# Kernel optimization log

Measured on AMD Instinct MI355X. Metric: run time of the kernel, lower is better.

The kernel has to match this reference:

```python
import jax, jax.numpy as jnp
import numpy as np

D_MODEL = 1024
N_HEADS = 16
HEAD_DIM = D_MODEL // N_HEADS
FFN = 4096
NUM_REL = 64
BATCH = 4
SEQ = 1024
EPS = 1e-6


def _layernorm(x, g, b):
    mu = jnp.mean(x, axis=-1, keepdims=True)
    var = jnp.mean(jnp.square(x - mu), axis=-1, keepdims=True)
    return (x - mu) * jax.lax.rsqrt(var + EPS) * g + b


def setup_inputs() -> dict:
    key = jax.random.key(0)
    ks = jax.random.split(key, 16)
    s_d = 1.0 / np.sqrt(D_MODEL)
    s_f = 1.0 / np.sqrt(FFN)
    inp = {
        "x": jax.random.normal(ks[0], (BATCH, SEQ, D_MODEL), jnp.float32),
        "relative_ids": jax.random.randint(ks[1], (SEQ, SEQ), 0, NUM_REL),
        # attention projections (row-major: y = x @ W + b)
        "Wq": jax.random.normal(ks[2], (D_MODEL, D_MODEL), jnp.float32) * s_d,
        "bq": jnp.zeros((D_MODEL,), jnp.float32),
        "Wk": jax.random.normal(ks[3], (D_MODEL, D_MODEL), jnp.float32) * s_d,
        "bk": jnp.zeros((D_MODEL,), jnp.float32),
        "Wv": jax.random.normal(ks[4], (D_MODEL, D_MODEL), jnp.float32) * s_d,
        "bv": jnp.zeros((D_MODEL,), jnp.float32),
        "Wo": jax.random.normal(ks[5], (D_MODEL, D_MODEL), jnp.float32) * s_d,
        "bo": jnp.zeros((D_MODEL,), jnp.float32),
        # relative position tables: Ek for keys (rel-e), Eb per-head bias (rel-b)
        "Ek": jax.random.normal(ks[6], (NUM_REL, HEAD_DIM), jnp.float32) * (1.0 / np.sqrt(HEAD_DIM)),
        "Eb": jax.random.normal(ks[7], (NUM_REL, N_HEADS), jnp.float32) * 0.02,
        # layernorms
        "g1": jnp.ones((D_MODEL,), jnp.float32),
        "b1": jnp.zeros((D_MODEL,), jnp.float32),
        "g2": jnp.ones((D_MODEL,), jnp.float32),
        "b2": jnp.zeros((D_MODEL,), jnp.float32),
        # FFN
        "W1": jax.random.normal(ks[8], (D_MODEL, FFN), jnp.float32) * s_d,
        "bf1": jnp.zeros((FFN,), jnp.float32),
        "W2": jax.random.normal(ks[9], (FFN, D_MODEL), jnp.float32) * s_f,
        "bf2": jnp.zeros((D_MODEL,), jnp.float32),
    }
    return inp


def _forward(x, relative_ids, Wq, bq, Wk, bk, Wv, bv, Wo, bo, Ek, Eb,
             g1, b1, g2, b2, W1, bf1, W2, bf2):
    B, S, D = x.shape
    # projections -> [B, H, S, Dh]
    def split_heads(t):
        return t.reshape(B, S, N_HEADS, HEAD_DIM).transpose(0, 2, 1, 3)
    q = split_heads(x @ Wq + bq)
    k = split_heads(x @ Wk + bk)
    v = split_heads(x @ Wv + bv)

    scores = jnp.einsum('bhqd,bhkd->bhqk', q, k)
    # rel-e: relative key embeddings interact with queries
    Erel = Ek[relative_ids]                      # [S, S, Dh]
    scores = scores + jnp.einsum('bhqd,qkd->bhqk', q, Erel)
    # rel-b: per-head relative bias
    scores = scores + Eb[relative_ids].transpose(2, 0, 1)[None]  # [1,H,S,S]
    scores = scores / jnp.sqrt(jnp.asarray(HEAD_DIM, x.dtype))

    attn = jax.nn.softmax(scores, axis=-1)
    ctx = jnp.einsum('bhqk,bhkd->bhqd', attn, v)
    ctx = ctx.transpose(0, 2, 1, 3).reshape(B, S, D)
    a_out = ctx @ Wo + bo

    # dropout is identity at eval
    ff_in = _layernorm(x + a_out, g1, b1)
    ff = jax.nn.relu(ff_in @ W1 + bf1) @ W2 + bf2
    return _layernorm(ff_in + ff, g2, b2)


def reference(x, relative_ids, Wq, bq, Wk, bk, Wv, bv, Wo, bo, Ek, Eb,
              g1, b1, g2, b2, W1, bf1, W2, bf2):
    return _forward(x, relative_ids, Wq, bq, Wk, bk, Wv, bv, Wo, bo, Ek, Eb,
                    g1, b1, g2, b2, W1, bf1, W2, bf2)
```

## Files before the change

### kernel.cpp

```cpp
#include <hip/hip_runtime.h>


typedef short bf16x8 __attribute__((ext_vector_type(8)));
typedef float f32x4 __attribute__((ext_vector_type(4)));

#define DEVI static __device__ __forceinline__

constexpr int SEQ = 1024, DMODEL = 1024, NH = 16, HDIM = 64, FFDIM = 4096, NREL = 64, NBATCH = 4;
constexpr int ROWS = NBATCH * SEQ;
#define QSC 0.18033688011112042f

DEVI unsigned short f2b(float f) {
  union { float f; unsigned u; } v; v.f = f;
  unsigned r = v.u + 0x7FFFu + ((v.u >> 16) & 1u);
  return (unsigned short)(r >> 16);
}

DEVI float b2f(unsigned short u) {
  union { unsigned v; float f; } x; x.v = (unsigned)u << 16; return x.f;
}

#if __has_builtin(__builtin_amdgcn_cvt_pk_bf16_f32)
DEVI unsigned pack2(float a, float b) {
  auto r = __builtin_amdgcn_cvt_pk_bf16_f32(a, b);
  return __builtin_bit_cast(unsigned, r);
}
#else
DEVI unsigned pack2(float a, float b) {
  return (unsigned)f2b(a) | ((unsigned)f2b(b) << 16);
}
#endif

DEVI float fexp2(float x) {
#if __has_builtin(__builtin_amdgcn_exp2f)
  return __builtin_amdgcn_exp2f(x);
#else
  return exp2f(x);
#endif
}

DEVI float4 ld4h(const unsigned short* p) {
  uint2 u = *(const uint2*)p;
  union { unsigned v; float f; } a, b, c, d;
  a.v = u.x << 16; b.v = u.x & 0xffff0000u; c.v = u.y << 16; d.v = u.y & 0xffff0000u;
  return make_float4(a.f, b.f, c.f, d.f);
}

DEVI void gload16(const unsigned short* g, unsigned short* l) {
  __builtin_amdgcn_global_load_lds((const __attribute__((address_space(1))) void*)g,
                                   (__attribute__((address_space(3))) void*)l, 16, 0, 0);
}

template <int BM, int BN>
DEVI void g256_core(const unsigned short* __restrict__ A, int lda,
                    const unsigned short* __restrict__ Bt, int ldb, int K,
                    unsigned short* S, f32x4* acc) {
  constexpr int MT = BM / 32, NT = BN / 64;
  constexpr int LOADS = BM / 64 + BN / 64;
  constexpr int SBUF = (BM + BN) * 64;
  const int tid = threadIdx.x, wave = tid >> 6, lane = tid & 63;
  const int wm = wave & 1, wn = wave >> 1;
  const int lr = lane & 15, kq = lane >> 4;
  const int srow = lane >> 3, schunk = (lane & 7) ^ (srow & 7);
  const int sw = lr & 7;

  const f32x4 zero = {0.f, 0.f, 0.f, 0.f};
#pragma unroll
  for (int i = 0; i < MT * NT; ++i) acc[i] = zero;

  const unsigned short* ga = A + (size_t)(wave * (BM / 8) + srow) * lda + schunk * 8;
  const unsigned short* gb = Bt + (size_t)(wave * (BN / 8) + srow) * ldb + schunk * 8;
  unsigned short* dA = S + wave * (BM / 8) * 64;
  unsigned short* dB = S + BM * 64 + wave * (BN / 8) * 64;

#define STG(buf, k0)                                                         \
  do {                                                                       \
    _Pragma("unroll") for (int j = 0; j < BM / 64; ++j)                      \
        gload16(ga + (size_t)(j * 8) * lda + (k0), dA + (buf)*SBUF + j * 8 * 64); \
    _Pragma("unroll") for (int j = 0; j < BN / 64; ++j)                      \
        gload16(gb + (size_t)(j * 8) * ldb + (k0), dB + (buf)*SBUF + j * 8 * 64); \
  } while (0)

  STG(0, 0);
  STG(1, 64);

  const unsigned short* pa = S + (wm * (BM / 2) + lr) * 64;
  const unsigned short* pb = S + BM * 64 + (wn * (BN / 4) + lr) * 64;
  const int nt = K >> 6;

  for (int t = 0; t < nt; ++t) {
    const int buf = t & 1;
    if (t < nt - 1) {
      if constexpr (LOADS == 8) {
        asm volatile("s_waitcnt vmcnt(8)" ::: "memory");
      } else {
        asm volatile("s_waitcnt vmcnt(6)" ::: "memory");
      }
    } else {
      asm volatile("s_waitcnt vmcnt(0)" ::: "memory");
    }
    __builtin_amdgcn_s_barrier();
    asm volatile("" ::: "memory");
    const unsigned short* qa = pa + buf * SBUF;
    const unsigned short* qb = pb + buf * SBUF;
#pragma unroll
    for (int ks = 0; ks < 2; ++ks) {
      const int rc = ((ks * 4 + kq) ^ sw) * 8;
      bf16x8 af[MT], bv[NT];
#pragma unroll
      for (int mi = 0; mi < MT; ++mi) af[mi] = *(const bf16x8*)(qa + mi * 16 * 64 + rc);
#pragma unroll
      for (int ni = 0; ni < NT; ++ni) bv[ni] = *(const bf16x8*)(qb + ni * 16 * 64 + rc);
#pragma unroll
      for (int mi = 0; mi < MT; ++mi)
#pragma unroll
        for (int ni = 0; ni < NT; ++ni)
          acc[mi * NT + ni] =
              __builtin_amdgcn_mfma_f32_16x16x32_bf16(af[mi], bv[ni], acc[mi * NT + ni], 0, 0, 0);
    }
    asm volatile("" ::: "memory");
    __builtin_amdgcn_s_barrier();
    asm volatile("" ::: "memory");
    if (t + 2 < nt) STG(buf, (t + 2) * 64);
  }
#undef STG
}

template <int BN2, bool RELU, bool SPLITK>
__global__ __launch_bounds__(512, 2) void k_g256(const unsigned short* __restrict__ A, int lda,
                                                 const unsigned short* __restrict__ Bt, int ldb,
                                                 int K, int N, const float* __restrict__ bias,
                                                 unsigned short* __restrict__ outh,
                                                 size_t ostride) {
  constexpr int BM = 256, MT = 8, NT = BN2 / 64;
  __shared__ __align__(16) unsigned short S[2 * (BM + BN2) * 64];
  f32x4 acc[MT * NT];
  const int m0 = blockIdx.y * BM, n0 = blockIdx.x * BN2;
  const int kc = SPLITK ? blockIdx.z : 0;
  g256_core<BM, BN2>(A + (size_t)m0 * lda + (size_t)kc * K, lda,
                     Bt + (size_t)n0 * ldb + (size_t)kc * K, ldb, K, S, acc);
  if (SPLITK) outh += (size_t)kc * ostride;
  const int tid = threadIdx.x, wave = tid >> 6, lane = tid & 63;
  const int wm = wave & 1, wn = wave >> 1, lr = lane & 15, kq = lane >> 4;
#pragma unroll
  for (int mi = 0; mi < MT; ++mi) {
    const int row0 = m0 + wm * 128 + mi * 16 + kq * 4;
#pragma unroll
    for (int ni = 0; ni < NT; ++ni) {
      const int col = n0 + wn * (BN2 / 4) + ni * 16 + lr;
      const float bc = (!SPLITK || kc == 0) ? bias[col] : 0.f;
      f32x4 v = acc[mi * NT + ni];
#pragma unroll
      for (int r = 0; r < 4; ++r) {
        float y = v[r] + bc;
        if (RELU) y = fmaxf(y, 0.f);
        outh[(size_t)(row0 + r) * N + col] = f2b(y);
      }
    }
  }
}

__global__ __launch_bounds__(512, 2) void k_proj256(
    const unsigned short* __restrict__ A, const unsigned short* __restrict__ WqT,
    const unsigned short* __restrict__ WkT, const unsigned short* __restrict__ WvT,
    const float* __restrict__ bq, const float* __restrict__ bk, const float* __restrict__ bv,
    unsigned short* __restrict__ oq, unsigned short* __restrict__ ok,
    unsigned short* __restrict__ ov) {
  __shared__ __align__(16) unsigned short S[2 * 512 * 64];
  f32x4 acc[32];
  const int which = blockIdx.z;
  const unsigned short* Bt = which == 0 ? WqT : which == 1 ? WkT : WvT;
  const float* bias = which == 0 ? bq : which == 1 ? bk : bv;
  unsigned short* out = which == 0 ? oq : which == 1 ? ok : ov;
  const float scl = which == 0 ? QSC : 1.0f;
  const int m0 = blockIdx.y * 256, n0 = blockIdx.x * 256;
  g256_core<256, 256>(A + (size_t)m0 * DMODEL, DMODEL, Bt + (size_t)n0 * DMODEL, DMODEL, DMODEL,
                      S, acc);
  const int tid = threadIdx.x, wave = tid >> 6, lane = tid & 63;
  const int wm = wave & 1, wn = wave >> 1, lr = lane & 15, kq = lane >> 4;
#pragma unroll
  for (int mi = 0; mi < 8; ++mi) {
    const int row0 = m0 + wm * 128 + mi * 16 + kq * 4;
    const int b = row0 >> 10, s0 = row0 & 1023;
#pragma unroll
    for (int ni = 0; ni < 4; ++ni) {
      const int col = n0 + wn * 64 + ni * 16 + lr;
      const int h = col >> 6, d = col & 63;
      const float bc = bias[col];
      f32x4 v = acc[mi * 4 + ni];
#pragma unroll
      for (int r = 0; r < 4; ++r) v[r] = (v[r] + bc) * scl;
      if (which != 2) {
#pragma unroll
        for (int r = 0; r < 4; ++r)
          out[((size_t)((b * NH + h) * SEQ) + s0 + r) * HDIM + d] = f2b(v[r]);
      } else {
        uint2 p = make_uint2(pack2(v[0], v[1]), pack2(v[2], v[3]));
        *(uint2*)&out[((size_t)((b * NH + h) * HDIM) + d) * SEQ + s0] = p;
      }
    }
  }
}

__global__ __launch_bounds__(256, 4) void k_flash(const unsigned short* __restrict__ q,
                                                  const unsigned short* __restrict__ kk,
                                                  const unsigned short* __restrict__ vT,
                                                  const unsigned short* __restrict__ Ekb,
                                                  const float* __restrict__ Eb,
                                                  const unsigned char* __restrict__ rel8,
                                                  unsigned short* __restrict__ ctx) {
  __shared__ __align__(16) unsigned short sK[128 * 64];
  __shared__ __align__(16) unsigned short sV[64 * 128];
  __shared__ __align__(16) unsigned short sqEB16[64 * 62];
  __shared__ float sRow[4][16];

  const int tid = threadIdx.x, wave = tid >> 6, lane = tid & 63;
  const int lr = lane & 15, kq = lane >> 4;

  const int L = blockIdx.y * 16 + blockIdx.x;
  const int xcd = L & 7, idx = L >> 3;
  const int z = xcd * 8 + (idx >> 4), qt = idx & 15;
  const int b = z >> 4, h = z & 15;
  const size_t zo = (size_t)z * SEQ * HDIM;
  const size_t vo = (size_t)z * HDIM * SEQ;

  const int srow8 = lane >> 3, sl8 = lane & 7;
  const int sw8 = sl8 ^ (srow8 & 7);
  const int dl = lane >> 4, sl16 = lane & 15;
  const int swl = lr & 7;
  const f32x4 zero = {0.f, 0.f, 0.f, 0.f};

  unsigned short* sQv = sV;
#pragma unroll
  for (int j = 0; j < 2; ++j) {
    const int row = wave * 16 + j * 8 + srow8;
    gload16(q + zo + (size_t)(qt * 64 + row) * 64 + sw8 * 8, sQv + (wave * 16 + j * 8) * 64);
    gload16(Ekb + (size_t)row * 64 + sw8 * 8, sK + (wave * 16 + j * 8) * 64);
  }
  __syncthreads();

  bf16x8 bq_[2];
#pragma unroll
  for (int ks = 0; ks < 2; ++ks)
    bq_[ks] = *(const bf16x8*)&sQv[(wave * 16 + lr) * 64 + (((ks * 4 + kq) ^ swl) << 3)];

  {
    f32x4 accE[4];
#pragma unroll
    for (int nf = 0; nf < 4; ++nf) accE[nf] = zero;
#pragma unroll
    for (int ks = 0; ks < 2; ++ks) {
#pragma unroll
      for (int nf = 0; nf < 4; ++nf) {
        bf16x8 ek = *(const bf16x8*)&sK[(nf * 16 + lr) * 64 + (((ks * 4 + kq) ^ swl) << 3)];
        accE[nf] = __builtin_amdgcn_mfma_f32_16x16x32_bf16(bq_[ks], ek, accE[nf], 0, 0, 0);
      }
    }
#pragma unroll
    for (int nf = 0; nf < 4; ++nf) {
      const int rid = nf * 16 + lr;
      const float eb = Eb[rid * NH + h] * QSC;
      const int base = rid * 62 + wave * 16 + kq * 4;
      *(unsigned*)&sqEB16[base] = pack2(accE[nf][0] + eb, accE[nf][1] + eb);
      *(unsigned*)&sqEB16[base + 2] = pack2(accE[nf][2] + eb, accE[nf][3] + eb);
    }
  }

  float l_run = 0.f;
  f32x4 accO[4];
#pragma unroll
  for (int nd = 0; nd < 4; ++nd) accO[nd] = zero;
  const int qrow_g = qt * 64 + wave * 16 + lr;
  const unsigned char* relrow8 = rel8 + (size_t)qrow_g * SEQ;
  const int qcol = wave * 16 + lr;
  unsigned short* sPw = sK + wave * 2048;

  for (int kt = 0; kt < 8; ++kt) {
    __syncthreads();
#pragma unroll
    for (int j = 0; j < 4; ++j) {
      const int row = wave * 32 + j * 8 + srow8;
      gload16(kk + zo + (size_t)(kt * 128 + row) * 64 + sw8 * 8, sK + (wave * 32 + j * 8) * 64);
    }
#pragma unroll
    for (int j = 0; j < 4; ++j) {
      const int row = wave * 16 + j * 4 + dl;
      const int ch = sl16 ^ (row & 15);
      gload16(vT + vo + (size_t)row * SEQ + kt * 128 + ch * 8, sV + (wave * 16 + j * 4) * 128);
    }
    unsigned ru[8];
#pragma unroll
    for (int mi = 0; mi < 8; ++mi)
      ru[mi] = *(const unsigned*)&relrow8[kt * 128 + mi * 16 + kq * 4];
    __syncthreads();

    f32x4 accS[8];
#pragma unroll
    for (int mi = 0; mi < 8; ++mi) accS[mi] = zero;
#pragma unroll
    for (int ks = 0; ks < 2; ++ks) {
#pragma unroll
      for (int mi = 0; mi < 8; ++mi) {
        bf16x8 a = *(const bf16x8*)&sK[(mi * 16 + lr) * 64 + (((ks * 4 + kq) ^ swl) << 3)];
        accS[mi] = __builtin_amdgcn_mfma_f32_16x16x32_bf16(a, bq_[ks], accS[mi], 0, 0, 0);
      }
    }
#pragma unroll
    for (int mi = 0; mi < 8; ++mi) {
      const float p0 = fexp2(accS[mi][0] + b2f(sqEB16[(int)(ru[mi] & 255u) * 62 + qcol]));
      const float p1 = fexp2(accS[mi][1] + b2f(sqEB16[(int)((ru[mi] >> 8) & 255u) * 62 + qcol]));
      const float p2 = fexp2(accS[mi][2] + b2f(sqEB16[(int)((ru[mi] >> 16) & 255u) * 62 + qcol]));
      const float p3 = fexp2(accS[mi][3] + b2f(sqEB16[(int)(ru[mi] >> 24) * 62 + qcol]));
      accS[mi][0] = p0; accS[mi][1] = p1; accS[mi][2] = p2; accS[mi][3] = p3;
      l_run += (p0 + p1) + (p2 + p3);
    }
    __syncthreads();

#pragma unroll
    for (int mi = 0; mi < 8; ++mi) {
      const int c = 2 * mi + (kq >> 1);
      *(uint2*)&sPw[lr * 128 + ((c ^ lr) << 3) + ((kq & 1) << 2)] =
          make_uint2(pack2(accS[mi][0], accS[mi][1]), pack2(accS[mi][2], accS[mi][3]));
    }
#pragma unroll
    for (int kst = 0; kst < 4; ++kst) {
      const int cc = ((kq + 4 * kst) ^ lr) << 3;
      bf16x8 a = *(const bf16x8*)&sPw[lr * 128 + cc];
#pragma unroll
      for (int nd = 0; nd < 4; ++nd) {
        bf16x8 bv = *(const bf16x8*)&sV[(nd * 16 + lr) * 128 + cc];
        accO[nd] = __builtin_amdgcn_mfma_f32_16x16x32_bf16(a, bv, accO[nd], 0, 0, 0);
      }
    }
  }

  l_run += __shfl_xor(l_run, 16);
  l_run += __shfl_xor(l_run, 32);
  if (kq == 0) sRow[wave][lr] = l_run;
  const float4 lv = *(const float4*)&sRow[wave][kq * 4];
  const float inv[4] = {1.f / lv.x, 1.f / lv.y, 1.f / lv.z, 1.f / lv.w};
  const size_t rbase = (size_t)(b * SEQ + qt * 64 + wave * 16 + kq * 4);
#pragma unroll
  for (int nd = 0; nd < 4; ++nd) {
    const int col = h * HDIM + nd * 16 + lr;
#pragma unroll
    for (int r = 0; r < 4; ++r)
      ctx[(rbase + r) * DMODEL + col] = f2b(accO[nd][r] * inv[r]);
  }
}

template <bool WB>
__global__ __launch_bounds__(256) void k_addln3(const unsigned short* __restrict__ a,
                                                const unsigned short* __restrict__ p0,
                                                const unsigned short* __restrict__ p1,
                                                const float* __restrict__ g,
                                                const float* __restrict__ beta,
                                                float* __restrict__ outf,
                                                unsigned short* __restrict__ outh) {
  const int row = blockIdx.x, t = threadIdx.x;
  const size_t base = (size_t)row * DMODEL + t * 4;
  float4 va = ld4h(&a[base]);
  float4 v0 = ld4h(&p0[base]);
  float4 v1 = ld4h(&p1[base]);
  const float x0 = va.x + v0.x + v1.x, x1 = va.y + v0.y + v1.y;
  const float x2 = va.z + v0.z + v1.z, x3 = va.w + v0.w + v1.w;
  __shared__ float red[4];
  float s = x0 + x1 + x2 + x3;
#pragma unroll
  for (int o = 32; o; o >>= 1) s += __shfl_xor(s, o);
  if ((t & 63) == 0) red[t >> 6] = s;
  __syncthreads();
  const float mu = (red[0] + red[1] + red[2] + red[3]) * (1.0f / DMODEL);
  __syncthreads();
  const float d0 = x0 - mu, d1 = x1 - mu, d2 = x2 - mu, d3 = x3 - mu;
  float qv = d0 * d0 + d1 * d1 + d2 * d2 + d3 * d3;
#pragma unroll
  for (int o = 32; o; o >>= 1) qv += __shfl_xor(qv, o);
  if ((t & 63) == 0) red[t >> 6] = qv;
  __syncthreads();
  const float var = (red[0] + red[1] + red[2] + red[3]) * (1.0f / DMODEL);
  const float sc = rsqrtf(var + 1e-6f);
  float4 vg = *(const float4*)&g[t * 4];
  float4 ve = *(const float4*)&beta[t * 4];
  float4 y;
  y.x = d0 * sc * vg.x + ve.x;
  y.y = d1 * sc * vg.y + ve.y;
  y.z = d2 * sc * vg.z + ve.z;
  y.w = d3 * sc * vg.w + ve.w;
  if (WB) {
    uint2 p = make_uint2(pack2(y.x, y.y), pack2(y.z, y.w));
    *(uint2*)&outh[base] = p;
  } else {
    *(float4*)&outf[base] = y;
  }
}

__global__ __launch_bounds__(256) void k_tcast12(
    const float* __restrict__ Wq, const float* __restrict__ Wk, const float* __restrict__ Wv,
    const float* __restrict__ Wo, const float* __restrict__ W1, const float* __restrict__ W2,
    unsigned short* __restrict__ oq, unsigned short* __restrict__ ok,
    unsigned short* __restrict__ ov, unsigned short* __restrict__ oo,
    unsigned short* __restrict__ o1, unsigned short* __restrict__ o2) {
  const int z = blockIdx.z;
  const float* in;
  unsigned short* out;
  int ldi, ldo;
  if (z < 4) {
    in = z == 0 ? Wq : z == 1 ? Wk : z == 2 ? Wv : Wo;
    out = z == 0 ? oq : z == 1 ? ok : z == 2 ? ov : oo;
    ldi = 1024; ldo = 1024;
  } else if (z < 8) {
    const int s = z - 4;
    in = W1 + (size_t)s * 1024; ldi = 4096;
    out = o1 + (size_t)s * 1024 * 1024; ldo = 1024;
  } else {
    const int s = z - 8;
    in = W2 + (size_t)s * 1024 * 1024; ldi = 1024;
    out = o2 + (size_t)s * 1024; ldo = 4096;
  }
  __shared__ float tile[32][33];
  const int tx = threadIdx.x & 31, ty = threadIdx.x >> 5;
  const int r0 = blockIdx.y * 32, c0 = blockIdx.x * 32;
#pragma unroll
  for (int i = 0; i < 4; ++i)
    tile[ty + i * 8][tx] = in[(size_t)(r0 + ty + i * 8) * ldi + c0 + tx];
  __syncthreads();
#pragma unroll
  for (int i = 0; i < 4; ++i)
    out[(size_t)(c0 + ty + i * 8) * ldo + r0 + tx] = f2b(tile[tx][ty + i * 8]);
}

__global__ __launch_bounds__(256) void k_cast2(const float* __restrict__ a,
                                               unsigned short* __restrict__ oa, int n4a,
                                               const float* __restrict__ bsrc,
                                               unsigned short* __restrict__ ob, int n4b,
                                               const int* __restrict__ rel,
                                               unsigned char* __restrict__ r8, int n4c) {
  const int i = blockIdx.x * 256 + threadIdx.x;
  if (i < n4a) {
    float4 v = *(const float4*)&a[(size_t)i * 4];
    uint2 p = make_uint2(pack2(v.x, v.y), pack2(v.z, v.w));
    *(uint2*)&oa[(size_t)i * 4] = p;
  } else {
    const int j = i - n4a;
    if (j < n4b) {
      float4 v = *(const float4*)&bsrc[(size_t)j * 4];
      uint2 p = make_uint2(pack2(v.x, v.y), pack2(v.z, v.w));
      *(uint2*)&ob[(size_t)j * 4] = p;
    } else {
      const int k2 = j - n4b;
      if (k2 < n4c) {
        int4 v = *(const int4*)&rel[(size_t)k2 * 4];
        unsigned pk = (unsigned)(v.x & 255) | ((unsigned)(v.y & 255) << 8) |
                      ((unsigned)(v.z & 255) << 16) | ((unsigned)(v.w & 255) << 24);
        *(unsigned*)&r8[(size_t)k2 * 4] = pk;
      }
    }
  }
}


extern "C" void kernel_launch(void* const* d_in, const int* in_sizes, int n_in, void* d_out,
                              int out_size, void* d_ws, size_t ws_size, hipStream_t stream) {
  const float* x = (const float*)d_in[0];
  const int* rel = (const int*)d_in[1];
  const float* Wq = (const float*)d_in[2];
  const float* bq = (const float*)d_in[3];
  const float* Wk = (const float*)d_in[4];
  const float* bk = (const float*)d_in[5];
  const float* Wv = (const float*)d_in[6];
  const float* bv = (const float*)d_in[7];
  const float* Wo = (const float*)d_in[8];
  const float* bo = (const float*)d_in[9];
  const float* Ek = (const float*)d_in[10];
  const float* Eb = (const float*)d_in[11];
  const float* g1 = (const float*)d_in[12];
  const float* b1 = (const float*)d_in[13];
  const float* g2 = (const float*)d_in[14];
  const float* b2 = (const float*)d_in[15];
  const float* W1 = (const float*)d_in[16];
  const float* bf1 = (const float*)d_in[17];
  const float* W2 = (const float*)d_in[18];
  const float* bf2 = (const float*)d_in[19];
  float* out = (float*)d_out;

  char* ws = (char*)d_ws;
  const size_t MB = 1ull << 20;
  unsigned short* Wqt = (unsigned short*)(ws + 0 * MB);
  unsigned short* Wkt = (unsigned short*)(ws + 2 * MB);
  unsigned short* Wvt = (unsigned short*)(ws + 4 * MB);
  unsigned short* Wot = (unsigned short*)(ws + 6 * MB);
  unsigned short* W1t = (unsigned short*)(ws + 8 * MB);
  unsigned short* W2t = (unsigned short*)(ws + 16 * MB);
  unsigned short* xb = (unsigned short*)(ws + 24 * MB);
  unsigned short* Ekb = (unsigned short*)(ws + 32 * MB);
  unsigned short* qbuf = (unsigned short*)(ws + 33 * MB);
  unsigned short* kbuf = (unsigned short*)(ws + 41 * MB);
  unsigned short* vTb = (unsigned short*)(ws + 49 * MB);
  unsigned short* ctx = (unsigned short*)(ws + 57 * MB);
  unsigned short* Pb = (unsigned short*)(ws + 65 * MB);
  unsigned char* rel8 = (unsigned char*)(ws + 65 * MB);
  unsigned short* ff_in_b = (unsigned short*)(ws + 81 * MB);
  unsigned short* hidden = (unsigned short*)(ws + 89 * MB);
  const size_t OST = (size_t)ROWS * DMODEL;

  k_tcast12<<<dim3(32, 32, 12), 256, 0, stream>>>(Wq, Wk, Wv, Wo, W1, W2, Wqt, Wkt, Wvt, Wot,
                                                  W1t, W2t);
  k_cast2<<<5124, 256, 0, stream>>>(x, xb, ROWS * DMODEL / 4, Ek, Ekb, NREL * HDIM / 4, rel, rel8,
                                    SEQ * SEQ / 4);

  k_proj256<<<dim3(4, 16, 3), 512, 0, stream>>>(xb, Wqt, Wkt, Wvt, bq, bk, bv, qbuf, kbuf, vTb);

  k_flash<<<dim3(16, 64), 256, 0, stream>>>(qbuf, kbuf, vTb, Ekb, Eb, rel8, ctx);

  k_g256<128, false, true><<<dim3(8, 16, 2), 512, 0, stream>>>(ctx, DMODEL, Wot, DMODEL,
                                                               DMODEL / 2, DMODEL, bo, Pb, OST);
  k_addln3<true><<<ROWS, 256, 0, stream>>>(xb, Pb, Pb + OST, g1, b1, nullptr, ff_in_b);

  k_g256<256, true, false><<<dim3(FFDIM / 256, ROWS / 256), 512, 0, stream>>>(
      ff_in_b, DMODEL, W1t, DMODEL, DMODEL, FFDIM, bf1, hidden, 0);
  k_g256<128, false, true><<<dim3(8, 16, 2), 512, 0, stream>>>(hidden, FFDIM, W2t, FFDIM,
                                                               FFDIM / 2, DMODEL, bf2, Pb, OST);
  k_addln3<false><<<ROWS, 256, 0, stream>>>(ff_in_b, Pb, Pb + OST, g2, b2, out, nullptr);
}
```

Before: 342.1 us.

## Pre-scale relative ids to byte offsets, add MFMA priority, split-K-4 on FFN down GEMM

The relative-id table is now stored as 16-bit values that are already scaled into byte offsets for the shared bias table. This removes the multiply-and-index work from the flash inner loop, but doubles the bytes read for rel ids. s_setprio is raised around the MFMA blocks in the attention kernel to favour matrix issue. The FFN down-projection changes from 2-way to 4-way split-K with 256-wide tiles, and a new add-layernorm kernel sums the four partials, trading more partial-sum traffic for better occupancy.

```diff
diff --git a/kernel.cpp b/kernel.cpp
--- a/kernel.cpp
+++ b/kernel.cpp
@@ -207,7 +207,7 @@
                                                   const unsigned short* __restrict__ vT,
                                                   const unsigned short* __restrict__ Ekb,
                                                   const float* __restrict__ Eb,
-                                                  const unsigned char* __restrict__ rel8,
+                                                  const unsigned short* __restrict__ rel16,
                                                   unsigned short* __restrict__ ctx) {
   __shared__ __align__(16) unsigned short sK[128 * 64];
   __shared__ __align__(16) unsigned short sV[64 * 128];
@@ -271,8 +271,9 @@
 #pragma unroll
   for (int nd = 0; nd < 4; ++nd) accO[nd] = zero;
   const int qrow_g = qt * 64 + wave * 16 + lr;
-  const unsigned char* relrow8 = rel8 + (size_t)qrow_g * SEQ;
+  const unsigned short* relrow16 = rel16 + (size_t)qrow_g * SEQ;
   const int qcol = wave * 16 + lr;
+  const char* sqb = (const char*)sqEB16 + 2 * qcol;
   unsigned short* sPw = sK + wave * 2048;
 
   for (int kt = 0; kt < 8; ++kt) {
@@ -288,15 +289,16 @@
       const int ch = sl16 ^ (row & 15);
       gload16(vT + vo + (size_t)row * SEQ + kt * 128 + ch * 8, sV + (wave * 16 + j * 4) * 128);
     }
-    unsigned ru[8];
+    uint2 ru[8];
 #pragma unroll
     for (int mi = 0; mi < 8; ++mi)
-      ru[mi] = *(const unsigned*)&relrow8[kt * 128 + mi * 16 + kq * 4];
+      ru[mi] = *(const uint2*)&relrow16[kt * 128 + mi * 16 + kq * 4];
     __syncthreads();
 
     f32x4 accS[8];
 #pragma unroll
     for (int mi = 0; mi < 8; ++mi) accS[mi] = zero;
+    __builtin_amdgcn_s_setprio(1);
 #pragma unroll
     for (int ks = 0; ks < 2; ++ks) {
 #pragma unroll
@@ -305,12 +307,13 @@
         accS[mi] = __builtin_amdgcn_mfma_f32_16x16x32_bf16(a, bq_[ks], accS[mi], 0, 0, 0);
       }
     }
+    __builtin_amdgcn_s_setprio(0);
 #pragma unroll
     for (int mi = 0; mi < 8; ++mi) {
-      const float p0 = fexp2(accS[mi][0] + b2f(sqEB16[(int)(ru[mi] & 255u) * 62 + qcol]));
-      const float p1 = fexp2(accS[mi][1] + b2f(sqEB16[(int)((ru[mi] >> 8) & 255u) * 62 + qcol]));
-      const float p2 = fexp2(accS[mi][2] + b2f(sqEB16[(int)((ru[mi] >> 16) & 255u) * 62 + qcol]));
-      const float p3 = fexp2(accS[mi][3] + b2f(sqEB16[(int)(ru[mi] >> 24) * 62 + qcol]));
+      const float p0 = fexp2(accS[mi][0] + b2f(*(const unsigned short*)(sqb + (ru[mi].x & 0xffffu))));
+      const float p1 = fexp2(accS[mi][1] + b2f(*(const unsigned short*)(sqb + (ru[mi].x >> 16))));
+      const float p2 = fexp2(accS[mi][2] + b2f(*(const unsigned short*)(sqb + (ru[mi].y & 0xffffu))));
+      const float p3 = fexp2(accS[mi][3] + b2f(*(const unsigned short*)(sqb + (ru[mi].y >> 16))));
       accS[mi][0] = p0; accS[mi][1] = p1; accS[mi][2] = p2; accS[mi][3] = p3;
       l_run += (p0 + p1) + (p2 + p3);
     }
@@ -322,6 +325,7 @@
       *(uint2*)&sPw[lr * 128 + ((c ^ lr) << 3) + ((kq & 1) << 2)] =
           make_uint2(pack2(accS[mi][0], accS[mi][1]), pack2(accS[mi][2], accS[mi][3]));
     }
+    __builtin_amdgcn_s_setprio(1);
 #pragma unroll
     for (int kst = 0; kst < 4; ++kst) {
       const int cc = ((kq + 4 * kst) ^ lr) << 3;
@@ -332,6 +336,7 @@
         accO[nd] = __builtin_amdgcn_mfma_f32_16x16x32_bf16(a, bv, accO[nd], 0, 0, 0);
       }
     }
+    __builtin_amdgcn_s_setprio(0);
   }
 
   l_run += __shfl_xor(l_run, 16);
@@ -393,6 +398,49 @@
   } else {
     *(float4*)&outf[base] = y;
   }
+}
+
+__global__ __launch_bounds__(256) void k_addln4(const unsigned short* __restrict__ a,
+                                                const unsigned short* __restrict__ p,
+                                                size_t ost,
+                                                const float* __restrict__ g,
+                                                const float* __restrict__ beta,
+                                                float* __restrict__ outf) {
+  const int row = blockIdx.x, t = threadIdx.x;
+  const size_t base = (size_t)row * DMODEL + t * 4;
+  float4 va = ld4h(&a[base]);
+  float4 v0 = ld4h(&p[base]);
+  float4 v1 = ld4h(&p[base + ost]);
+  float4 v2 = ld4h(&p[base + 2 * ost]);
+  float4 v3 = ld4h(&p[base + 3 * ost]);
+  const float x0 = va.x + (v0.x + v1.x) + (v2.x + v3.x);
+  const float x1 = va.y + (v0.y + v1.y) + (v2.y + v3.y);
+  const float x2 = va.z + (v0.z + v1.z) + (v2.z + v3.z);
+  const float x3 = va.w + (v0.w + v1.w) + (v2.w + v3.w);
+  __shared__ float red[4];
+  float s = x0 + x1 + x2 + x3;
+#pragma unroll
+  for (int o = 32; o; o >>= 1) s += __shfl_xor(s, o);
+  if ((t & 63) == 0) red[t >> 6] = s;
+  __syncthreads();
+  const float mu = (red[0] + red[1] + red[2] + red[3]) * (1.0f / DMODEL);
+  __syncthreads();
+  const float d0 = x0 - mu, d1 = x1 - mu, d2 = x2 - mu, d3 = x3 - mu;
+  float qv = d0 * d0 + d1 * d1 + d2 * d2 + d3 * d3;
+#pragma unroll
+  for (int o = 32; o; o >>= 1) qv += __shfl_xor(qv, o);
+  if ((t & 63) == 0) red[t >> 6] = qv;
+  __syncthreads();
+  const float var = (red[0] + red[1] + red[2] + red[3]) * (1.0f / DMODEL);
+  const float sc = rsqrtf(var + 1e-6f);
+  float4 vg = *(const float4*)&g[t * 4];
+  float4 ve = *(const float4*)&beta[t * 4];
+  float4 y;
+  y.x = d0 * sc * vg.x + ve.x;
+  y.y = d1 * sc * vg.y + ve.y;
+  y.z = d2 * sc * vg.z + ve.z;
+  y.w = d3 * sc * vg.w + ve.w;
+  *(float4*)&outf[base] = y;
 }
 
 __global__ __launch_bounds__(256) void k_tcast12(
@@ -435,7 +483,7 @@
                                                const float* __restrict__ bsrc,
                                                unsigned short* __restrict__ ob, int n4b,
                                                const int* __restrict__ rel,
-                                               unsigned char* __restrict__ r8, int n4c) {
+                                               unsigned short* __restrict__ r16, int n4c) {
   const int i = blockIdx.x * 256 + threadIdx.x;
   if (i < n4a) {
     float4 v = *(const float4*)&a[(size_t)i * 4];
@@ -451,9 +499,10 @@
       const int k2 = j - n4b;
       if (k2 < n4c) {
         int4 v = *(const int4*)&rel[(size_t)k2 * 4];
-        unsigned pk = (unsigned)(v.x & 255) | ((unsigned)(v.y & 255) << 8) |
-                      ((unsigned)(v.z & 255) << 16) | ((unsigned)(v.w & 255) << 24);
-        *(unsigned*)&r8[(size_t)k2 * 4] = pk;
+        uint2 pk;
+        pk.x = (unsigned)((v.x & 63) * 124) | ((unsigned)((v.y & 63) * 124) << 16);
+        pk.y = (unsigned)((v.z & 63) * 124) | ((unsigned)((v.w & 63) * 124) << 16);
+        *(uint2*)&r16[(size_t)k2 * 4] = pk;
       }
     }
   }
@@ -499,19 +548,20 @@
   unsigned short* vTb = (unsigned short*)(ws + 49 * MB);
   unsigned short* ctx = (unsigned short*)(ws + 57 * MB);
   unsigned short* Pb = (unsigned short*)(ws + 65 * MB);
-  unsigned char* rel8 = (unsigned char*)(ws + 65 * MB);
+  unsigned short* rel16 = (unsigned short*)(ws + 65 * MB);
+  unsigned short* Pb4 = (unsigned short*)(ws + 33 * MB);
   unsigned short* ff_in_b = (unsigned short*)(ws + 81 * MB);
   unsigned short* hidden = (unsigned short*)(ws + 89 * MB);
   const size_t OST = (size_t)ROWS * DMODEL;
 
   k_tcast12<<<dim3(32, 32, 12), 256, 0, stream>>>(Wq, Wk, Wv, Wo, W1, W2, Wqt, Wkt, Wvt, Wot,
                                                   W1t, W2t);
-  k_cast2<<<5124, 256, 0, stream>>>(x, xb, ROWS * DMODEL / 4, Ek, Ekb, NREL * HDIM / 4, rel, rel8,
-                                    SEQ * SEQ / 4);
+  k_cast2<<<5124, 256, 0, stream>>>(x, xb, ROWS * DMODEL / 4, Ek, Ekb, NREL * HDIM / 4, rel,
+                                    rel16, SEQ * SEQ / 4);
 
   k_proj256<<<dim3(4, 16, 3), 512, 0, stream>>>(xb, Wqt, Wkt, Wvt, bq, bk, bv, qbuf, kbuf, vTb);
 
-  k_flash<<<dim3(16, 64), 256, 0, stream>>>(qbuf, kbuf, vTb, Ekb, Eb, rel8, ctx);
+  k_flash<<<dim3(16, 64), 256, 0, stream>>>(qbuf, kbuf, vTb, Ekb, Eb, rel16, ctx);
 
   k_g256<128, false, true><<<dim3(8, 16, 2), 512, 0, stream>>>(ctx, DMODEL, Wot, DMODEL,
                                                                DMODEL / 2, DMODEL, bo, Pb, OST);
@@ -519,7 +569,7 @@
 
   k_g256<256, true, false><<<dim3(FFDIM / 256, ROWS / 256), 512, 0, stream>>>(
       ff_in_b, DMODEL, W1t, DMODEL, DMODEL, FFDIM, bf1, hidden, 0);
-  k_g256<128, false, true><<<dim3(8, 16, 2), 512, 0, stream>>>(hidden, FFDIM, W2t, FFDIM,
-                                                               FFDIM / 2, DMODEL, bf2, Pb, OST);
-  k_addln3<false><<<ROWS, 256, 0, stream>>>(ff_in_b, Pb, Pb + OST, g2, b2, out, nullptr);
-}
+  k_g256<256, false, true><<<dim3(4, 16, 4), 512, 0, stream>>>(hidden, FFDIM, W2t, FFDIM,
+                                                               FFDIM / 4, DMODEL, bf2, Pb4, OST);
+  k_addln4<<<ROWS, 256, 0, stream>>>(ff_in_b, Pb4, OST, g2, b2, out);
+}
```

Measured after the change: 348.9 us. About the same (+2.0%).
